# Performance work log

Hardware: AMD Instinct MI355X
Metric: run time of the kernel (lower is better)

## Reference

```python
import jax, jax.numpy as jnp
import numpy as np

TAU_MIN = 0.001
XPBD_ITERS = 4
XPBD_COMPLIANCE = 0.0
XPBD_MAX_CORR = 0.15

B, N, D, E = 4, 50000, 256, 800000


def setup_inputs() -> dict:
    key = jax.random.key(0)
    ks = jax.random.split(key, 7)
    keypoints = jax.random.normal(ks[0], (B, N, 3), dtype=jnp.float32)
    timesteps = jax.random.uniform(ks[1], (B,), dtype=jnp.float32)
    hand_tokens = jax.random.normal(ks[2], (B, N, D), dtype=jnp.float32)
    head_w = jax.random.normal(ks[3], (D, 3), dtype=jnp.float32) * 0.02
    head_b = jnp.zeros((3,), dtype=jnp.float32)
    edge_index = jax.random.randint(ks[4], (2, E), 0, N, dtype=jnp.int32)
    rest_lengths = jax.random.uniform(ks[5], (E,), dtype=jnp.float32) + 0.1
    return {
        "keypoints": keypoints,
        "timesteps": timesteps,
        "hand_tokens": hand_tokens,
        "head_w": head_w,
        "head_b": head_b,
        "edge_index": edge_index,
        "rest_lengths": rest_lengths,
    }


def _xpbd_project(x, src, dst, rest_lengths):
    # x: (B, N, 3); src/dst: (E,); rest_lengths: (E,)
    L0 = rest_lengths[None, :, None]          # (1, E, 1)
    w_i = 1.0                                  # inv_mass is None -> unit inverse masses
    w_j = 1.0
    alpha = XPBD_COMPLIANCE / (float(XPBD_ITERS) + 1e-08)
    denom = w_i + w_j + alpha + 1e-09
    for _ in range(XPBD_ITERS):
        diff = x[:, src] - x[:, dst]           # (B, E, 3) edge gather
        dist = jnp.linalg.norm(diff, axis=-1, keepdims=True)  # (B, E, 1)
        C = dist - L0
        n = diff / (dist + 1e-09)
        d_lambda = -C / denom
        correction = jnp.clip(d_lambda * n, -XPBD_MAX_CORR, XPBD_MAX_CORR)
        delta = (jnp.zeros_like(x)
                 .at[:, src].add(w_i * correction)
                 .at[:, dst].add(-w_j * correction))  # scatter-add back to nodes
        x = x + delta
    return x


def reference(keypoints, timesteps, hand_tokens, head_w, head_b, edge_index, rest_lengths):
    # tau = clamp(1 - t, min=tau_min), broadcast to (B, 1, 1)
    tau = jnp.maximum(1.0 - timesteps, TAU_MIN)[:, None, None]
    v_raw = hand_tokens @ head_w + head_b      # (B, N, 3) velocity head
    x_pred = keypoints + tau * v_raw
    src = edge_index[0]
    dst = edge_index[1]
    x_corrected = _xpbd_project(x_pred, src, dst, rest_lengths)
    v_eff = (x_corrected - keypoints) / tau
    return v_eff
```

## Files before the change

### kernel.cpp

```cpp
#include <hip/hip_runtime.h>

#define BB 4
#define NN 50000
#define DD 256
#define EE 800000
#define TAU_MIN_F 0.001f
#define MAX_CORR_F 0.15f

#define CAP 80
#define NPART 8
#define PNODES (NN / NPART)
#define PS_CE 2048
#define PS_NCHUNK ((EE + PS_CE - 1) / PS_CE)

__global__ __launch_bounds__(256) void xpred_kernel(
    const float* __restrict__ kp, const float* __restrict__ ts,
    const float* __restrict__ ht, const float* __restrict__ hw,
    const float* __restrict__ hb, float4* __restrict__ x)
{
    const int lane  = threadIdx.x & 63;
    const int wave  = (blockIdx.x * blockDim.x + threadIdx.x) >> 6;
    const int nwave = (gridDim.x * blockDim.x) >> 6;

    const int d0 = lane * 4;
    float W[4][3];
#pragma unroll
    for (int j = 0; j < 4; ++j)
#pragma unroll
        for (int k = 0; k < 3; ++k)
            W[j][k] = hw[(d0 + j) * 3 + k];
    const float b0 = hb[0], b1 = hb[1], b2 = hb[2];

    for (int i = wave; i < BB * NN; i += nwave) {
        const int node = i >> 2;
        const int b    = i & 3;
        const int row  = b * NN + node;
        const float4 h = *(const float4*)(ht + (size_t)row * DD + d0);
        float a0 = h.x * W[0][0] + h.y * W[1][0] + h.z * W[2][0] + h.w * W[3][0];
        float a1 = h.x * W[0][1] + h.y * W[1][1] + h.z * W[2][1] + h.w * W[3][1];
        float a2 = h.x * W[0][2] + h.y * W[1][2] + h.z * W[2][2] + h.w * W[3][2];
#pragma unroll
        for (int off = 32; off > 0; off >>= 1) {
            a0 += __shfl_down(a0, off);
            a1 += __shfl_down(a1, off);
            a2 += __shfl_down(a2, off);
        }
        if (lane == 0) {
            const float tau = fmaxf(1.0f - ts[b], TAU_MIN_F);
            float4 v;
            v.x = kp[row * 3 + 0] + tau * (a0 + b0);
            v.y = kp[row * 3 + 1] + tau * (a1 + b1);
            v.z = kp[row * 3 + 2] + tau * (a2 + b2);
            v.w = 0.0f;
            x[i] = v;
        }
    }
}

__global__ __launch_bounds__(256) void pbucket_kernel(
    const int* __restrict__ ei, const float* __restrict__ L0,
    int* __restrict__ counts, int2* __restrict__ adj)
{
    const int lo   = (int)blockIdx.x * PNODES;
    const int hi   = lo + PNODES;
    const int base = (int)blockIdx.y * PS_CE;
    const int eEnd = min(base + PS_CE, EE);
    for (int e = base + (int)threadIdx.x; e < eEnd; e += 256) {
        const int s = ei[e];
        const int d = ei[EE + e];
        const int r = __float_as_int(L0[e]);
        if (s >= lo && s < hi) {
            const int p = atomicAdd(&counts[s], 1);
            if (p < CAP) adj[s * CAP + p] = make_int2(d, r);
        }
        if (d >= lo && d < hi) {
            const int p = atomicAdd(&counts[d], 1);
            if (p < CAP) adj[d * CAP + p] = make_int2(s, r);
        }
    }
}

__global__ __launch_bounds__(256) void gather_kernel(
    const float4* __restrict__ xin, float4* __restrict__ xout,
    const int* __restrict__ counts, const int2* __restrict__ adj,
    const float* __restrict__ kp, const float* __restrict__ ts,
    float* __restrict__ out, int final_iter)
{
    const int tid  = blockIdx.x * 256 + threadIdx.x;
    const int b    = tid & 3;
    const int sub  = (tid >> 2) & 3;
    const int node = tid >> 4;

    const float4 xc = xin[(node << 2) + b];
    float a0 = 0.0f, a1 = 0.0f, a2 = 0.0f;

    const int beg = node * CAP;
    const int end = beg + min(counts[node], CAP);

    int k = beg + sub;
    for (; k + 4 < end; k += 8) {
        const int2 e0 = adj[k];
        const int2 e1 = adj[k + 4];
        const float4 n0 = xin[(e0.x << 2) + b];
        const float4 n1 = xin[(e1.x << 2) + b];
        {
            const float dx = xc.x - n0.x, dy = xc.y - n0.y, dz = xc.z - n0.z;
            const float dist = sqrtf(dx * dx + dy * dy + dz * dz);
            const float s = (__int_as_float(e0.y) - dist) * 0.5f / (dist + 1e-9f);
            a0 += fminf(fmaxf(s * dx, -MAX_CORR_F), MAX_CORR_F);
            a1 += fminf(fmaxf(s * dy, -MAX_CORR_F), MAX_CORR_F);
            a2 += fminf(fmaxf(s * dz, -MAX_CORR_F), MAX_CORR_F);
        }
        {
            const float dx = xc.x - n1.x, dy = xc.y - n1.y, dz = xc.z - n1.z;
            const float dist = sqrtf(dx * dx + dy * dy + dz * dz);
            const float s = (__int_as_float(e1.y) - dist) * 0.5f / (dist + 1e-9f);
            a0 += fminf(fmaxf(s * dx, -MAX_CORR_F), MAX_CORR_F);
            a1 += fminf(fmaxf(s * dy, -MAX_CORR_F), MAX_CORR_F);
            a2 += fminf(fmaxf(s * dz, -MAX_CORR_F), MAX_CORR_F);
        }
    }
    if (k < end) {
        const int2 e0 = adj[k];
        const float4 n0 = xin[(e0.x << 2) + b];
        const float dx = xc.x - n0.x, dy = xc.y - n0.y, dz = xc.z - n0.z;
        const float dist = sqrtf(dx * dx + dy * dy + dz * dz);
        const float s = (__int_as_float(e0.y) - dist) * 0.5f / (dist + 1e-9f);
        a0 += fminf(fmaxf(s * dx, -MAX_CORR_F), MAX_CORR_F);
        a1 += fminf(fmaxf(s * dy, -MAX_CORR_F), MAX_CORR_F);
        a2 += fminf(fmaxf(s * dz, -MAX_CORR_F), MAX_CORR_F);
    }

    a0 += __shfl_xor(a0, 4);  a0 += __shfl_xor(a0, 8);
    a1 += __shfl_xor(a1, 4);  a1 += __shfl_xor(a1, 8);
    a2 += __shfl_xor(a2, 4);  a2 += __shfl_xor(a2, 8);

    if (sub == 0) {
        if (!final_iter) {
            float4 v; v.x = xc.x + a0; v.y = xc.y + a1; v.z = xc.z + a2; v.w = 0.0f;
            xout[(node << 2) + b] = v;
        } else {
            const int row = b * NN + node;
            const float tau = fmaxf(1.0f - ts[b], TAU_MIN_F);
            const float it  = 1.0f / tau;
            out[row * 3 + 0] = (xc.x + a0 - kp[row * 3 + 0]) * it;
            out[row * 3 + 1] = (xc.y + a1 - kp[row * 3 + 1]) * it;
            out[row * 3 + 2] = (xc.z + a2 - kp[row * 3 + 2]) * it;
        }
    }
}

extern "C" void kernel_launch(void* const* d_in, const int* in_sizes, int n_in,
                              void* d_out, int out_size, void* d_ws, size_t ws_size,
                              hipStream_t stream)
{
    const float* kp = (const float*)d_in[0];
    const float* ts = (const float*)d_in[1];
    const float* ht = (const float*)d_in[2];
    const float* hw = (const float*)d_in[3];
    const float* hb = (const float*)d_in[4];
    const int*   ei = (const int*)d_in[5];
    const float* L0 = (const float*)d_in[6];
    float* out = (float*)d_out;

    char* w = (char*)d_ws;
    int2*   adj    = (int2*)w;                 w += (size_t)NN * CAP * sizeof(int2);
    float4* xA     = (float4*)w;               w += (size_t)BB * NN * sizeof(float4);
    float4* xB     = (float4*)w;               w += (size_t)BB * NN * sizeof(float4);
    int*    counts = (int*)w;

    hipMemsetAsync(counts, 0, (size_t)NN * sizeof(int), stream);

    xpred_kernel<<<1024, 256, 0, stream>>>(kp, ts, ht, hw, hb, xA);

    pbucket_kernel<<<dim3(NPART, PS_NCHUNK), 256, 0, stream>>>(ei, L0, counts, adj);

    const int gatherBlocks = (16 * NN) / 256;
    gather_kernel<<<gatherBlocks, 256, 0, stream>>>(xA, xB, counts, adj, kp, ts, out, 0);
    gather_kernel<<<gatherBlocks, 256, 0, stream>>>(xB, xA, counts, adj, kp, ts, out, 0);
    gather_kernel<<<gatherBlocks, 256, 0, stream>>>(xA, xB, counts, adj, kp, ts, out, 0);
    gather_kernel<<<gatherBlocks, 256, 0, stream>>>(xB, xA, counts, adj, kp, ts, out, 1);
}
```

Baseline: 461.4 us.

## Fuse projection and bucketing into one kernel, widen gather to 8 lanes per node

```diff
diff --git a/kernel.cpp b/kernel.cpp
--- a/kernel.cpp
+++ b/kernel.cpp
@@ -13,16 +13,45 @@
 #define PS_CE 2048
 #define PS_NCHUNK ((EE + PS_CE - 1) / PS_CE)
 
-__global__ __launch_bounds__(256) void xpred_kernel(
+#define XPB 2048
+#define S1_GRID (XPB + NPART * PS_NCHUNK)
+#define NWAVE (XPB * 4)
+
+__global__ __launch_bounds__(256) void stage1_kernel(
     const float* __restrict__ kp, const float* __restrict__ ts,
     const float* __restrict__ ht, const float* __restrict__ hw,
-    const float* __restrict__ hb, float4* __restrict__ x)
+    const float* __restrict__ hb, float4* __restrict__ x,
+    const int* __restrict__ ei, const float* __restrict__ L0,
+    int* __restrict__ counts, int2* __restrict__ adj)
 {
-    const int lane  = threadIdx.x & 63;
-    const int wave  = (blockIdx.x * blockDim.x + threadIdx.x) >> 6;
-    const int nwave = (gridDim.x * blockDim.x) >> 6;
-
-    const int d0 = lane * 4;
+    if ((int)blockIdx.x >= XPB) {
+        const int pb    = (int)blockIdx.x - XPB;
+        const int part  = pb & 7;
+        const int chunk = pb >> 3;
+        const int lo   = part * PNODES;
+        const int hi   = lo + PNODES;
+        const int base = chunk * PS_CE;
+        const int eEnd = min(base + PS_CE, EE);
+        for (int e = base + (int)threadIdx.x; e < eEnd; e += 256) {
+            const int s = ei[e];
+            const int d = ei[EE + e];
+            const int r = __float_as_int(L0[e]);
+            if (s >= lo && s < hi) {
+                const int p = atomicAdd(&counts[s], 1);
+                if (p < CAP) adj[s * CAP + p] = make_int2(d << 2, r);
+            }
+            if (d >= lo && d < hi) {
+                const int p = atomicAdd(&counts[d], 1);
+                if (p < CAP) adj[d * CAP + p] = make_int2(s << 2, r);
+            }
+        }
+        return;
+    }
+
+    const int lane = threadIdx.x & 63;
+    const int wave = ((int)blockIdx.x * 256 + (int)threadIdx.x) >> 6;
+    const int d0   = lane * 4;
+
     float W[4][3];
 #pragma unroll
     for (int j = 0; j < 4; ++j)
@@ -31,10 +60,53 @@
             W[j][k] = hw[(d0 + j) * 3 + k];
     const float b0 = hb[0], b1 = hb[1], b2 = hb[2];
 
-    for (int i = wave; i < BB * NN; i += nwave) {
-        const int node = i >> 2;
-        const int b    = i & 3;
-        const int row  = b * NN + node;
+    int i = wave;
+    for (; i + NWAVE < BB * NN; i += 2 * NWAVE) {
+        const int iA = i, iB = i + NWAVE;
+        const int rowA = (iA & 3) * NN + (iA >> 2);
+        const int rowB = (iB & 3) * NN + (iB >> 2);
+        const float4 hA = *(const float4*)(ht + (size_t)rowA * DD + d0);
+        const float4 hB = *(const float4*)(ht + (size_t)rowB * DD + d0);
+        float aA0 = hA.x * W[0][0] + hA.y * W[1][0] + hA.z * W[2][0] + hA.w * W[3][0];
+        float aA1 = hA.x * W[0][1] + hA.y * W[1][1] + hA.z * W[2][1] + hA.w * W[3][1];
+        float aA2 = hA.x * W[0][2] + hA.y * W[1][2] + hA.z * W[2][2] + hA.w * W[3][2];
+        float aB0 = hB.x * W[0][0] + hB.y * W[1][0] + hB.z * W[2][0] + hB.w * W[3][0];
+        float aB1 = hB.x * W[0][1] + hB.y * W[1][1] + hB.z * W[2][1] + hB.w * W[3][1];
+        float aB2 = hB.x * W[0][2] + hB.y * W[1][2] + hB.z * W[2][2] + hB.w * W[3][2];
+#pragma unroll
+        for (int off = 32; off > 0; off >>= 1) {
+            aA0 += __shfl_down(aA0, off);
+            aB0 += __shfl_down(aB0, off);
+            aA1 += __shfl_down(aA1, off);
+            aB1 += __shfl_down(aB1, off);
+            aA2 += __shfl_down(aA2, off);
+            aB2 += __shfl_down(aB2, off);
+        }
+        if (lane == 0) {
+            {
+                const int bA = iA & 3;
+                const float tau = fmaxf(1.0f - ts[bA], TAU_MIN_F);
+                float4 v;
+                v.x = kp[rowA * 3 + 0] + tau * (aA0 + b0);
+                v.y = kp[rowA * 3 + 1] + tau * (aA1 + b1);
+                v.z = kp[rowA * 3 + 2] + tau * (aA2 + b2);
+                v.w = 0.0f;
+                x[iA] = v;
+            }
+            {
+                const int bB = iB & 3;
+                const float tau = fmaxf(1.0f - ts[bB], TAU_MIN_F);
+                float4 v;
+                v.x = kp[rowB * 3 + 0] + tau * (aB0 + b0);
+                v.y = kp[rowB * 3 + 1] + tau * (aB1 + b1);
+                v.z = kp[rowB * 3 + 2] + tau * (aB2 + b2);
+                v.w = 0.0f;
+                x[iB] = v;
+            }
+        }
+    }
+    if (i < BB * NN) {
+        const int row = (i & 3) * NN + (i >> 2);
         const float4 h = *(const float4*)(ht + (size_t)row * DD + d0);
         float a0 = h.x * W[0][0] + h.y * W[1][0] + h.z * W[2][0] + h.w * W[3][0];
         float a1 = h.x * W[0][1] + h.y * W[1][1] + h.z * W[2][1] + h.w * W[3][1];
@@ -46,6 +118,7 @@
             a2 += __shfl_down(a2, off);
         }
         if (lane == 0) {
+            const int b = i & 3;
             const float tau = fmaxf(1.0f - ts[b], TAU_MIN_F);
             float4 v;
             v.x = kp[row * 3 + 0] + tau * (a0 + b0);
@@ -53,29 +126,6 @@
             v.z = kp[row * 3 + 2] + tau * (a2 + b2);
             v.w = 0.0f;
             x[i] = v;
-        }
-    }
-}
-
-__global__ __launch_bounds__(256) void pbucket_kernel(
-    const int* __restrict__ ei, const float* __restrict__ L0,
-    int* __restrict__ counts, int2* __restrict__ adj)
-{
-    const int lo   = (int)blockIdx.x * PNODES;
-    const int hi   = lo + PNODES;
-    const int base = (int)blockIdx.y * PS_CE;
-    const int eEnd = min(base + PS_CE, EE);
-    for (int e = base + (int)threadIdx.x; e < eEnd; e += 256) {
-        const int s = ei[e];
-        const int d = ei[EE + e];
-        const int r = __float_as_int(L0[e]);
-        if (s >= lo && s < hi) {
-            const int p = atomicAdd(&counts[s], 1);
-            if (p < CAP) adj[s * CAP + p] = make_int2(d, r);
-        }
-        if (d >= lo && d < hi) {
-            const int p = atomicAdd(&counts[d], 1);
-            if (p < CAP) adj[d * CAP + p] = make_int2(s, r);
         }
     }
 }
@@ -88,8 +138,8 @@
 {
     const int tid  = blockIdx.x * 256 + threadIdx.x;
     const int b    = tid & 3;
-    const int sub  = (tid >> 2) & 3;
-    const int node = tid >> 4;
+    const int sub  = (tid >> 2) & 7;
+    const int node = tid >> 5;
 
     const float4 xc = xin[(node << 2) + b];
     float a0 = 0.0f, a1 = 0.0f, a2 = 0.0f;
@@ -98,11 +148,11 @@
     const int end = beg + min(counts[node], CAP);
 
     int k = beg + sub;
-    for (; k + 4 < end; k += 8) {
+    for (; k + 8 < end; k += 16) {
         const int2 e0 = adj[k];
-        const int2 e1 = adj[k + 4];
-        const float4 n0 = xin[(e0.x << 2) + b];
-        const float4 n1 = xin[(e1.x << 2) + b];
+        const int2 e1 = adj[k + 8];
+        const float4 n0 = xin[e0.x + b];
+        const float4 n1 = xin[e1.x + b];
         {
             const float dx = xc.x - n0.x, dy = xc.y - n0.y, dz = xc.z - n0.z;
             const float dist = sqrtf(dx * dx + dy * dy + dz * dz);
@@ -122,7 +172,7 @@
     }
     if (k < end) {
         const int2 e0 = adj[k];
-        const float4 n0 = xin[(e0.x << 2) + b];
+        const float4 n0 = xin[e0.x + b];
         const float dx = xc.x - n0.x, dy = xc.y - n0.y, dz = xc.z - n0.z;
         const float dist = sqrtf(dx * dx + dy * dy + dz * dz);
         const float s = (__int_as_float(e0.y) - dist) * 0.5f / (dist + 1e-9f);
@@ -131,9 +181,9 @@
         a2 += fminf(fmaxf(s * dz, -MAX_CORR_F), MAX_CORR_F);
     }
 
-    a0 += __shfl_xor(a0, 4);  a0 += __shfl_xor(a0, 8);
-    a1 += __shfl_xor(a1, 4);  a1 += __shfl_xor(a1, 8);
-    a2 += __shfl_xor(a2, 4);  a2 += __shfl_xor(a2, 8);
+    a0 += __shfl_xor(a0, 4);  a0 += __shfl_xor(a0, 8);  a0 += __shfl_xor(a0, 16);
+    a1 += __shfl_xor(a1, 4);  a1 += __shfl_xor(a1, 8);  a1 += __shfl_xor(a1, 16);
+    a2 += __shfl_xor(a2, 4);  a2 += __shfl_xor(a2, 8);  a2 += __shfl_xor(a2, 16);
 
     if (sub == 0) {
         if (!final_iter) {
@@ -171,11 +221,10 @@
 
     hipMemsetAsync(counts, 0, (size_t)NN * sizeof(int), stream);
 
-    xpred_kernel<<<1024, 256, 0, stream>>>(kp, ts, ht, hw, hb, xA);
-
-    pbucket_kernel<<<dim3(NPART, PS_NCHUNK), 256, 0, stream>>>(ei, L0, counts, adj);
-
-    const int gatherBlocks = (16 * NN) / 256;
+    stage1_kernel<<<S1_GRID, 256, 0, stream>>>(kp, ts, ht, hw, hb, xA,
+                                               ei, L0, counts, adj);
+
+    const int gatherBlocks = (32 * NN) / 256;
     gather_kernel<<<gatherBlocks, 256, 0, stream>>>(xA, xB, counts, adj, kp, ts, out, 0);
     gather_kernel<<<gatherBlocks, 256, 0, stream>>>(xB, xA, counts, adj, kp, ts, out, 0);
     gather_kernel<<<gatherBlocks, 256, 0, stream>>>(xA, xB, counts, adj, kp, ts, out, 0);
```

Result: faster. 438.6 us (-4.9%).
